# Kernel tuning notes

Hardware: AMD Instinct MI355X
Metric: run time of the kernel (lower is better)

Reference implementation:

```python
import jax, jax.numpy as jnp
import numpy as np

HID = 256

def lstm_cell(x, h, c, Wih, Whh, bih, bhh):
    # PyTorch LSTM gate order: i, f, g, o
    g = x @ Wih.T + h @ Whh.T + bih + bhh
    i, f, gg, o = jnp.split(g, 4, axis=-1)
    c = jax.nn.sigmoid(f) * c + jax.nn.sigmoid(i) * jnp.tanh(gg)
    h = jax.nn.sigmoid(o) * jnp.tanh(c)
    return h, c

def lstm_seq(x, Wih, Whh, bih, bhh):
    # x: [B, T, D] -> outputs [B, T, H], final (h, c)
    B = x.shape[0]
    h0 = jnp.zeros((B, HID), x.dtype)
    def step(carry, xt):
        h, c = lstm_cell(xt, carry[0], carry[1], Wih, Whh, bih, bhh)
        return (h, c), h
    (h, c), ys = jax.lax.scan(step, (h0, h0), jnp.swapaxes(x, 0, 1))
    return jnp.swapaxes(ys, 0, 1), h, c

def setup_inputs():
    key = jax.random.key(0)
    B, M, H_WIN, NTH, NTW = 512, 16, 25, 64, 64
    SAL = NTH * NTW
    ks = iter(jax.random.split(key, 40))
    def U(shape):
        return jax.random.uniform(next(ks), shape, jnp.float32, -0.0625, 0.0625)
    def lstm_p(pfx, din):
        return {pfx + '_Wih': U((4 * HID, din)), pfx + '_Whh': U((4 * HID, HID)),
                pfx + '_bih': U((4 * HID,)), pfx + '_bhh': U((4 * HID,))}
    inp = {
        'encoder_position_inputs': jax.random.normal(next(ks), (B, M, 3), jnp.float32) * 0.1,
        'encoder_saliency_inputs': jax.random.uniform(next(ks), (B, M, NTH, NTW), jnp.float32),
        'decoder_position_inputs': jax.random.normal(next(ks), (B, 1, 3), jnp.float32) * 0.1,
        'decoder_saliency_inputs': jax.random.uniform(next(ks), (B, H_WIN, NTH, NTW), jnp.float32),
    }
    for pfx, din in [('pe', 3), ('se', SAL), ('fe', 2 * HID), ('pd', 3), ('sd', SAL), ('fd', 2 * HID)]:
        inp.update(lstm_p(pfx, din))
    inp['f2_W'] = U((HID, HID)); inp['f2_b'] = U((HID,))
    inp['out_W'] = U((3, HID)); inp['out_b'] = U((3,))
    return inp

def reference(encoder_position_inputs, encoder_saliency_inputs, decoder_position_inputs, decoder_saliency_inputs,
              pe_Wih, pe_Whh, pe_bih, pe_bhh, se_Wih, se_Whh, se_bih, se_bhh,
              fe_Wih, fe_Whh, fe_bih, fe_bhh, pd_Wih, pd_Whh, pd_bih, pd_bhh,
              sd_Wih, sd_Whh, sd_bih, sd_bhh, fd_Wih, fd_Whh, fd_bih, fd_bhh,
              f2_W, f2_b, out_W, out_b):
    B, M = encoder_position_inputs.shape[:2]
    SAL = encoder_saliency_inputs.shape[2] * encoder_saliency_inputs.shape[3]
    # encoder
    out_pos, h1, c1 = lstm_seq(encoder_position_inputs, pe_Wih, pe_Whh, pe_bih, pe_bhh)
    out_sal, h2, c2 = lstm_seq(encoder_saliency_inputs.reshape(B, M, SAL), se_Wih, se_Whh, se_bih, se_bhh)
    conc_enc = jnp.concatenate([out_sal, out_pos], axis=-1)
    _, hf, cf = lstm_seq(conc_enc, fe_Wih, fe_Whh, fe_bih, fe_bhh)
    # decoder: H_WINDOW single-step recurrence; fuse LSTM restarts from (hf, cf) every step
    dec_sal = decoder_saliency_inputs.reshape(B, -1, SAL)
    def step(carry, sal_t):
        inp, h1, c1, h2, c2 = carry
        h1, c1 = lstm_cell(inp, h1, c1, pd_Wih, pd_Whh, pd_bih, pd_bhh)
        h2, c2 = lstm_cell(sal_t, h2, c2, sd_Wih, sd_Whh, sd_bih, sd_bhh)
        conc = jnp.concatenate([h2, h1], axis=-1)
        hfd, _ = lstm_cell(conc, hf, cf, fd_Wih, fd_Whh, fd_bih, fd_bhh)
        fuse2 = hfd @ f2_W.T + f2_b
        delta = fuse2 @ out_W.T + out_b
        pred = inp + delta  # toPosition: orientation + motion
        return (pred, h1, c1, h2, c2), pred
    init = (decoder_position_inputs[:, 0], h1, c1, h2, c2)
    _, preds = jax.lax.scan(step, init, jnp.swapaxes(dec_sal, 0, 1))
    return jnp.swapaxes(preds, 0, 1)  # [B, H_WINDOW, 3]
```

## Files before the change

### kernel.cpp

```cpp
#include <hip/hip_runtime.h>

#define HID 256
#define BATCH 512
#define MENC 16
#define HWIN 25
#define SALSZ 4096
#define BH (BATCH * HID)

typedef __attribute__((ext_vector_type(8))) short bf16x8;
typedef __attribute__((ext_vector_type(4))) float f32x4;

__device__ __forceinline__ float sigmf(float x) { return 1.0f / (1.0f + __expf(-x)); }
__device__ __forceinline__ ushort f2bf(float f) {
    uint32_t u = __float_as_uint(f);
    return (ushort)((u + 0x7fffu + ((u >> 16) & 1u)) >> 16);
}

#define GLOAD_LDS(gp, lp) \
    __builtin_amdgcn_global_load_lds((const __attribute__((address_space(1))) void*)(gp), \
                                     (__attribute__((address_space(3))) void*)(lp), 16, 0, 0)

__device__ __forceinline__ void st_u64(void* p, unsigned long long v) {
    __hip_atomic_store((unsigned long long*)p, v, __ATOMIC_RELAXED, __HIP_MEMORY_SCOPE_AGENT);
}

__device__ __forceinline__ void gbar_arrive(unsigned int* slot)
{
    __syncthreads();
    if (threadIdx.x == 0) atomicAdd(slot, 1u);
}
__device__ __forceinline__ void gbar_wait(unsigned int* slot, unsigned int nblk)
{
    if (threadIdx.x == 0) {
        while (__hip_atomic_load(slot, __ATOMIC_RELAXED, __HIP_MEMORY_SCOPE_AGENT) < nblk)
            __builtin_amdgcn_s_sleep(1);
    }
    __syncthreads();
}

__device__ __forceinline__ void stage_wtile(const ushort* Wsrc, int ldw, int u0,
                                            ushort* lds, int lane, int wq)
{
    const int sub = lane >> 5, uu = lane & 31;
#pragma unroll
    for (int i = 0; i < 8; ++i) {
        const int row = i * 8 + wq * 2 + sub;
        const int su  = uu ^ (row & 7);
        const int gr  = (row >> 4) * HID + u0 + (row & 15);
        GLOAD_LDS(Wsrc + (size_t)gr * ldw + su * 8, lds + i * 2048 + wq * 512);
    }
}

__device__ __forceinline__ void cell_g(const ushort* hrow0, int ldh,
                                       const ushort* WsL, f32x4 acc[4], int lane)
{
    const int fr = lane & 15, fq = lane >> 4;
    const ushort* hrow = hrow0 + (size_t)fr * ldh;
#pragma unroll
    for (int ks = 0; ks < 8; ++ks) {
        const bf16x8 af = *(const bf16x8*)(hrow + ks * 32 + fq * 8);
#pragma unroll
        for (int g = 0; g < 4; ++g) {
            const int vr = g * 16 + fr;
            const bf16x8 bf = *(const bf16x8*)(WsL + vr * 256 + (((ks * 4 + fq)) ^ (vr & 7)) * 8);
            acc[g] = __builtin_amdgcn_mfma_f32_16x16x32_bf16(af, bf, acc[g], 0, 0, 0);
        }
    }
}

struct Cvt9 {
    const float* s[9];
    ushort*      d[9];
    int          end[9];
};
__global__ __launch_bounds__(256)
void cvt_multi(Cvt9 A)
{
    int i = blockIdx.x * 256 + threadIdx.x;
    if (i >= A.end[8]) return;
    int seg = 0, beg = 0;
#pragma unroll
    for (int k = 0; k < 8; ++k)
        if (i >= A.end[k]) { seg = k + 1; beg = A.end[k]; }
    const int j = i - beg;
    const float4 v = *(const float4*)(A.s[seg] + (size_t)j * 4);
    *(ushort4*)(A.d[seg] + (size_t)j * 4) = make_ushort4(f2bf(v.x), f2bf(v.y), f2bf(v.z), f2bf(v.w));
}

__device__ __forceinline__ void loadA_f32(const float* Ag, int lda, int tid, float4 a[8])
{
    const int row_in = tid >> 3, ulin = tid & 7;
#pragma unroll
    for (int i = 0; i < 4; ++i) {
        const int row = i * 64 + row_in;
        const int su = (ulin ^ (row & 7)) * 8;
        a[2 * i + 0] = *(const float4*)(Ag + (size_t)row * lda + su);
        a[2 * i + 1] = *(const float4*)(Ag + (size_t)row * lda + su + 4);
    }
}
__device__ __forceinline__ void writeA_bf16(const float4 a[8], ushort* Al, int tid)
{
    const int row_in = tid >> 3, ulin = tid & 7;
#pragma unroll
    for (int i = 0; i < 4; ++i) {
        const int row = i * 64 + row_in;
        uint4 v;
        v.x = (uint)f2bf(a[2 * i].x) | ((uint)f2bf(a[2 * i].y) << 16);
        v.y = (uint)f2bf(a[2 * i].z) | ((uint)f2bf(a[2 * i].w) << 16);
        v.z = (uint)f2bf(a[2 * i + 1].x) | ((uint)f2bf(a[2 * i + 1].y) << 16);
        v.w = (uint)f2bf(a[2 * i + 1].z) | ((uint)f2bf(a[2 * i + 1].w) << 16);
        *(uint4*)(Al + row * 64 + ulin * 8) = v;
    }
}
__device__ __forceinline__ void stageB(const ushort* Bg, int ldw, ushort* Bl, int tid)
{
    const int row_in = tid >> 3, ulin = tid & 7;
#pragma unroll
    for (int i = 0; i < 4; ++i) {
        const int row = i * 64 + row_in;
        const int su = (ulin ^ (row & 7)) * 8;
        GLOAD_LDS(Bg + (size_t)row * ldw + su, Bl + row * 64 + ulin * 8);
    }
}

struct GemmJob { const float* A; const ushort* W; float* C; int nwg; };

__global__ __launch_bounds__(512, 2)
void gemm256f2(GemmJob j0, GemmJob j1)
{
    __shared__ ushort As[2][256 * 64];
    __shared__ ushort Bs[2][256 * 64];
    const int tid = threadIdx.x, lane = tid & 63, wid = tid >> 6;

    const GemmJob J = (blockIdx.x < (unsigned)j0.nwg) ? j0 : j1;
    int bid = (blockIdx.x < (unsigned)j0.nwg) ? blockIdx.x : blockIdx.x - j0.nwg;
    {
        const int nwg = J.nwg, q = nwg >> 3, r = nwg & 7;
        const int xcd = bid & 7, o = bid >> 3;
        bid = (xcd < r) ? xcd * (q + 1) + o : r * (q + 1) + (xcd - r) * q + o;
    }
    const int gx = 4;
    const int m0 = (bid / gx) * 256, n0 = (bid % gx) * 256;
    const int lda = SALSZ, ldw = SALSZ, ldc = 1024, K = SALSZ;

    const int wr = wid >> 2, wc = wid & 3;
    const int fr = lane & 15, fq = lane >> 4;

    f32x4 acc[8][4] = {};
    const int nt = K / 64;
    const float*  Ab0 = J.A + (size_t)m0 * lda;
    const ushort* Bb0 = J.W + (size_t)n0 * ldw;

    float4 ra[8];
    loadA_f32(Ab0, lda, tid, ra);
    stageB(Bb0, ldw, Bs[0], tid);
    writeA_bf16(ra, As[0], tid);
    loadA_f32(Ab0 + 64, lda, tid, ra);
    asm volatile("s_waitcnt vmcnt(8) lgkmcnt(0)" ::: "memory");
    __builtin_amdgcn_sched_barrier(0);
    __builtin_amdgcn_s_barrier();
    __builtin_amdgcn_sched_barrier(0);

    for (int t = 0; t < nt; ++t) {
        const int p = t & 1;
        const int t1 = (t + 1 < nt) ? t + 1 : nt - 1;
        const int t2 = (t + 2 < nt) ? t + 2 : nt - 1;
        stageB(Bb0 + t1 * 64, ldw, Bs[p ^ 1], tid);
        writeA_bf16(ra, As[p ^ 1], tid);
        loadA_f32(Ab0 + t2 * 64, lda, tid, ra);

        const ushort* Ab = As[p];
        const ushort* Bb = Bs[p];
#pragma unroll
        for (int ks = 0; ks < 2; ++ks) {
            bf16x8 bfr[4];
#pragma unroll
            for (int nf = 0; nf < 4; ++nf) {
                const int row = wc * 64 + nf * 16 + fr;
                bfr[nf] = *(const bf16x8*)(Bb + row * 64 + ((ks * 4 + fq) ^ (row & 7)) * 8);
            }
#pragma unroll
            for (int mh = 0; mh < 2; ++mh) {
                bf16x8 af[4];
#pragma unroll
                for (int i = 0; i < 4; ++i) {
                    const int row = wr * 128 + (mh * 4 + i) * 16 + fr;
                    af[i] = *(const bf16x8*)(Ab + row * 64 + ((ks * 4 + fq) ^ (row & 7)) * 8);
                }
                __builtin_amdgcn_s_setprio(1);
#pragma unroll
                for (int i = 0; i < 4; ++i)
#pragma unroll
                    for (int nf = 0; nf < 4; ++nf)
                        acc[mh * 4 + i][nf] = __builtin_amdgcn_mfma_f32_16x16x32_bf16(
                            af[i], bfr[nf], acc[mh * 4 + i][nf], 0, 0, 0);
                __builtin_amdgcn_s_setprio(0);
            }
        }
        if (t == nt - 1) break;
        asm volatile("s_waitcnt vmcnt(8) lgkmcnt(0)" ::: "memory");
        __builtin_amdgcn_sched_barrier(0);
        __builtin_amdgcn_s_barrier();
        __builtin_amdgcn_sched_barrier(0);
    }

    const int cl = lane & 15, ch = lane >> 4;
#pragma unroll
    for (int mf = 0; mf < 8; ++mf)
#pragma unroll
        for (int nf = 0; nf < 4; ++nf)
#pragma unroll
            for (int r = 0; r < 4; ++r)
                J.C[(size_t)(m0 + wr * 128 + mf * 16 + ch * 4 + r) * ldc
                    + n0 + wc * 64 + nf * 16 + cl] = acc[mf][nf][r];
}

__global__ __launch_bounds__(256)
void gemm_mfma_bt(const ushort* __restrict__ A, const ushort* __restrict__ W,
                  float* __restrict__ C, int M, int N, int K,
                  int lda, int ldw, int ldc, const float* __restrict__ rbias)
{
    __shared__ ushort As[128 * 32];
    __shared__ ushort Bs[128 * 32];
    const int t    = threadIdx.x;
    const int lane = t & 63, wid = t >> 6;
    const int m0 = blockIdx.y * 128, n0 = blockIdx.x * 128;
    const int wr = wid >> 1, wc = wid & 1;

    f32x4 acc[4][4] = {};

    const int sr = wid * 16 + (lane >> 2);
    const int su = ((lane & 3) ^ ((lane >> 3) & 3)) * 8;
    const ushort* Ag = A + (size_t)(m0 + sr) * lda + su;
    const ushort* Wg = W + (size_t)(n0 + sr) * ldw + su;
    ushort* Al = As + wid * 512;
    ushort* Bl = Bs + wid * 512;

    const int fr = lane & 15;
    const int fq = lane >> 4;
    const int sw = (fr >> 1) & 3;

    for (int k0 = 0; k0 < K; k0 += 32) {
        GLOAD_LDS(Ag,                    Al);
        GLOAD_LDS(Ag + (size_t)64 * lda, Al + 2048);
        GLOAD_LDS(Wg,                    Bl);
        GLOAD_LDS(Wg + (size_t)64 * ldw, Bl + 2048);
        Ag += 32; Wg += 32;
        __syncthreads();

        bf16x8 af[4], bfr[4];
#pragma unroll
        for (int m = 0; m < 4; ++m)
            af[m] = *(const bf16x8*)(As + (wr * 64 + m * 16 + fr) * 32 + (fq ^ sw) * 8);
#pragma unroll
        for (int n = 0; n < 4; ++n)
            bfr[n] = *(const bf16x8*)(Bs + (wc * 64 + n * 16 + fr) * 32 + (fq ^ sw) * 8);
#pragma unroll
        for (int m = 0; m < 4; ++m)
#pragma unroll
            for (int n = 0; n < 4; ++n)
                acc[m][n] = __builtin_amdgcn_mfma_f32_16x16x32_bf16(af[m], bfr[n], acc[m][n], 0, 0, 0);
        __syncthreads();
    }

    const int cl = lane & 15, ch = lane >> 4;
#pragma unroll
    for (int m = 0; m < 4; ++m)
#pragma unroll
        for (int n = 0; n < 4; ++n)
#pragma unroll
            for (int r = 0; r < 4; ++r) {
                const int mm = m0 + wr * 64 + m * 16 + ch * 4 + r;
                const int nn = n0 + wc * 64 + n * 16 + cl;
                float v = acc[m][n][r];
                if (rbias) v += rbias[(size_t)(mm & 511) * ldc + nn];
                C[(size_t)mm * ldc + nn] = v;
            }
}

__global__ __launch_bounds__(256)
void gemm_tn(const float* __restrict__ A, const float* __restrict__ W,
             const float* __restrict__ b1, const float* __restrict__ b2,
             float* __restrict__ C,
             int M, int N, int K, int lda, int ldw, int ldc)
{
    __shared__ float AsT[16][68];
    __shared__ float WsT[16][68];
    const int t  = threadIdx.x;
    const int tx = t & 15, ty = t >> 4;
    const int m0 = blockIdx.y * 64, n0 = blockIdx.x * 64;
    const int lr = t >> 2;
    const int c4 = t & 3;

    float acc[4][4];
#pragma unroll
    for (int i = 0; i < 4; ++i)
#pragma unroll
        for (int j = 0; j < 4; ++j) acc[i][j] = 0.0f;

    for (int k0 = 0; k0 < K; k0 += 16) {
        float a[4], w[4];
        const int kb = k0 + c4 * 4;
#pragma unroll
        for (int k = 0; k < 4; ++k) {
            a[k] = (kb + k < K) ? A[(size_t)(m0 + lr) * lda + kb + k] : 0.0f;
            w[k] = (kb + k < K) ? W[(size_t)(n0 + lr) * ldw + kb + k] : 0.0f;
        }
        __syncthreads();
#pragma unroll
        for (int k = 0; k < 4; ++k) {
            AsT[c4 * 4 + k][lr] = a[k];
            WsT[c4 * 4 + k][lr] = w[k];
        }
        __syncthreads();
#pragma unroll
        for (int kk = 0; kk < 16; ++kk) {
            const float4 av = *(const float4*)&AsT[kk][ty * 4];
            const float4 wv = *(const float4*)&WsT[kk][tx * 4];
            acc[0][0] += av.x * wv.x; acc[0][1] += av.x * wv.y; acc[0][2] += av.x * wv.z; acc[0][3] += av.x * wv.w;
            acc[1][0] += av.y * wv.x; acc[1][1] += av.y * wv.y; acc[1][2] += av.y * wv.z; acc[1][3] += av.y * wv.w;
            acc[2][0] += av.z * wv.x; acc[2][1] += av.z * wv.y; acc[2][2] += av.z * wv.z; acc[2][3] += av.z * wv.w;
            acc[3][0] += av.w * wv.x; acc[3][1] += av.w * wv.y; acc[3][2] += av.w * wv.z; acc[3][3] += av.w * wv.w;
        }
    }

#pragma unroll
    for (int i = 0; i < 4; ++i) {
        const int m = m0 + ty * 4 + i;
#pragma unroll
        for (int j = 0; j < 4; ++j) {
            const int n = n0 + tx * 4 + j;
            float v = acc[i][j];
            if (b1) v += b1[n];
            if (b2) v += b2[n];
            C[(size_t)m * ldc + n] = v;
        }
    }
}

struct EncArgs {
    const ushort *WHse, *WHpe;
    const float  *xg_se;
    const float  *enc_pos;
    const float  *se_b1, *se_b2, *pe_b1, *pe_b2;
    const float  *pe_Wih;
    ushort       *conc;
    float        *SE_C, *PE_C;
    unsigned int *bar;
};

__global__ __launch_bounds__(1024)
void enc_chain(EncArgs A)
{
    __shared__ ushort Ws[4][64 * 256];
    __shared__ ushort hloc[64][64];
    const int tid = threadIdx.x, lane = tid & 63, w = tid >> 6;
    const int role  = blockIdx.x >> 5;
    const int rem   = blockIdx.x & 31;
    const int btile = rem & 7, usup = rem >> 3;
    const int b0 = btile * 64, ub = usup * 64;
    const int usub = w & 3, bsub = w >> 2;
    const int u0t = ub + usub * 16;
    const int grp = role * 8 + btile;
    const int fr = lane & 15, fq = lane >> 4;
    const int u = u0t + fr;
    const int ul = usub * 16 + fr;
    const int coff = role ? 256 : 0;

    stage_wtile(role ? A.WHpe : A.WHse, HID, u0t, Ws[usub], lane, bsub);

    const float* b1 = role ? A.pe_b1 : A.se_b1;
    const float* b2 = role ? A.pe_b2 : A.se_b2;
    float bias[4], wxs[4][3];
#pragma unroll
    for (int g = 0; g < 4; ++g) {
        bias[g] = b1[g * HID + u] + b2[g * HID + u];
        wxs[g][0] = wxs[g][1] = wxs[g][2] = 0.0f;
        if (role) {
            wxs[g][0] = A.pe_Wih[(g * HID + u) * 3 + 0];
            wxs[g][1] = A.pe_Wih[(g * HID + u) * 3 + 1];
            wxs[g][2] = A.pe_Wih[(g * HID + u) * 3 + 2];
        }
    }
    float c[4] = {0.f, 0.f, 0.f, 0.f};
    __syncthreads();

    for (int t = 0; t < MENC; ++t) {
        float xg[4][4];
#pragma unroll
        for (int r = 0; r < 4; ++r) {
            const int b = b0 + bsub * 16 + fq * 4 + r;
            if (role) {
                const float* xp = A.enc_pos + ((size_t)b * MENC + t) * 3;
                xg[r][0] = xp[0]; xg[r][1] = xp[1]; xg[r][2] = xp[2]; xg[r][3] = 0.f;
            } else {
#pragma unroll
                for (int g = 0; g < 4; ++g)
                    xg[r][g] = A.xg_se[((size_t)b * MENC + t) * 1024 + g * HID + u];
            }
        }
        if (t > 0) gbar_wait(A.bar + grp * MENC + (t - 1), 4);
        f32x4 acc[4] = {};
        if (t > 0)
            cell_g(A.conc + ((size_t)(t - 1) * 512 + b0 + bsub * 16) * 512 + coff, 512,
                   Ws[usub], acc, lane);
#pragma unroll
        for (int r = 0; r < 4; ++r) {
            const int bl = bsub * 16 + fq * 4 + r;
            const int b = b0 + bl;
            float gv[4];
#pragma unroll
            for (int g = 0; g < 4; ++g) {
                float v = acc[g][r] + bias[g];
                if (role) v += xg[r][0] * wxs[g][0] + xg[r][1] * wxs[g][1] + xg[r][2] * wxs[g][2];
                else      v += xg[r][g];
                gv[g] = v;
            }
            const float cn = sigmf(gv[1]) * c[r] + sigmf(gv[0]) * tanhf(gv[2]);
            const float hn = sigmf(gv[3]) * tanhf(cn);
            c[r] = cn;
            hloc[bl][ul] = f2bf(hn);
            if (t == MENC - 1) (role ? A.PE_C : A.SE_C)[(size_t)b * HID + u] = cn;
        }
        __syncthreads();
        {
            const int row = tid >> 4, c8 = tid & 15;
            const unsigned long long v = *(const unsigned long long*)&hloc[row][c8 * 4];
            st_u64(A.conc + ((size_t)t * 512 + b0 + row) * 512 + coff + ub + c8 * 4, v);
        }
        if (t != MENC - 1) gbar_arrive(A.bar + grp * MENC + t);
    }
}

struct MidArgs {
    const ushort *WHsd, *WHfe;
    const float  *xg_sd;
    const float  *xg_fe;
    const float  *sd_b1, *sd_b2, *fe_b1, *fe_b2;
    const ushort *conc;
    const float  *SE_C;
    ushort       *SDB;
    ushort       *FEB;
    float        *FEH, *FE_C;
    unsigned int *bar;
};

__global__ __launch_bounds__(1024)
void mid_chain(MidArgs A)
{
    __shared__ ushort Ws[4][64 * 256];
    __shared__ ushort hloc[64][64];
    const int tid = threadIdx.x, lane = tid & 63, w = tid >> 6;
    const int role  = blockIdx.x >> 5;
    const int rem   = blockIdx.x & 31;
    const int btile = rem & 7, usup = rem >> 3;
    const int b0 = btile * 64, ub = usup * 64;
    const int usub = w & 3, bsub = w >> 2;
    const int u0t = ub + usub * 16;
    const int grp = role * 8 + btile;
    const int fr = lane & 15, fq = lane >> 4;
    const int u = u0t + fr;
    const int ul = usub * 16 + fr;
    const int NT = role ? MENC : HWIN;

    stage_wtile(role ? A.WHfe : A.WHsd, HID, u0t, Ws[usub], lane, bsub);

    const float* b1 = role ? A.fe_b1 : A.sd_b1;
    const float* b2 = role ? A.fe_b2 : A.sd_b2;
    float bias[4];
#pragma unroll
    for (int g = 0; g < 4; ++g) bias[g] = b1[g * HID + u] + b2[g * HID + u];

    float c[4];
#pragma unroll
    for (int r = 0; r < 4; ++r) {
        const int b = b0 + bsub * 16 + fq * 4 + r;
        c[r] = role ? 0.0f : A.SE_C[(size_t)b * HID + u];
    }
    __syncthreads();

    for (int t = 0; t < NT; ++t) {
        float xg[4][4];
#pragma unroll
        for (int r = 0; r < 4; ++r) {
            const int b = b0 + bsub * 16 + fq * 4 + r;
#pragma unroll
            for (int g = 0; g < 4; ++g)
                xg[r][g] = role ? A.xg_fe[((size_t)t * 512 + b) * 1024 + g * HID + u]
                                : A.xg_sd[((size_t)b * HWIN + t) * 1024 + g * HID + u];
        }
        if (t > 0) gbar_wait(A.bar + grp * HWIN + (t - 1), 4);
        f32x4 acc[4] = {};
        if (role == 0) {
            if (t == 0) cell_g(A.conc + ((size_t)15 * 512 + b0 + bsub * 16) * 512, 512,
                               Ws[usub], acc, lane);
            else        cell_g(A.SDB + ((size_t)(t - 1) * 512 + b0 + bsub * 16) * HID, HID,
                               Ws[usub], acc, lane);
        } else if (t > 0) {
            cell_g(A.FEB + ((size_t)(t - 1) * BATCH + b0 + bsub * 16) * HID, HID,
                   Ws[usub], acc, lane);
        }
#pragma unroll
        for (int r = 0; r < 4; ++r) {
            const int bl = bsub * 16 + fq * 4 + r;
            const int b = b0 + bl;
            float gv[4];
#pragma unroll
            for (int g = 0; g < 4; ++g)
                gv[g] = acc[g][r] + bias[g] + xg[r][g];
            const float cn = sigmf(gv[1]) * c[r] + sigmf(gv[0]) * tanhf(gv[2]);
            const float hn = sigmf(gv[3]) * tanhf(cn);
            c[r] = cn;
            hloc[bl][ul] = f2bf(hn);
            if (role == 1 && t == MENC - 1) {
                A.FEH[(size_t)b * HID + u] = hn;
                A.FE_C[(size_t)b * HID + u] = cn;
            }
        }
        __syncthreads();
        {
            const int row = tid >> 4, c8 = tid & 15;
            const unsigned long long v = *(const unsigned long long*)&hloc[row][c8 * 4];
            ushort* dst = role ? (A.FEB + ((size_t)t * BATCH + b0 + row) * 256 + ub + c8 * 4)
                               : (A.SDB + ((size_t)t * 512 + b0 + row) * 256 + ub + c8 * 4);
            st_u64(dst, v);
        }
        if (t != NT - 1) gbar_arrive(A.bar + grp * HWIN + t);
    }
}

struct DecArgs {
    const ushort *WHpd;
    const ushort *WFDh;
    const ushort *peF;
    const float  *PE_C, *FE_C;
    const float  *xh2;
    const float  *pd_b1, *pd_b2, *pd_Wih;
    const float  *G, *c3, *dec_pos;
    ushort       *H1;
    float        *DELTA;
    float        *out;
    unsigned int *bar;
};

__global__ __launch_bounds__(512)
void dec_chain(DecArgs A)
{
    __shared__ ushort Wpd[2][64 * 256], Wfd[2][64 * 256];
    __shared__ ushort hloc[64][32];
    __shared__ float pred_lds[192];
    const int tid = threadIdx.x, lane = tid & 63, w = tid >> 6;
    const int btile = blockIdx.x & 7, usup = blockIdx.x >> 3;
    const int b0 = btile * 64, ub = usup * 32;
    const int usub = w & 1, bsub = w >> 1;
    const int u0t = ub + usub * 16;
    const int fr = lane & 15, fq = lane >> 4;
    const int u = u0t + fr;
    const int ul = usub * 16 + fr;
    unsigned int* bars = A.bar + btile * 2 * HWIN;

    stage_wtile(A.WHpd, HID, u0t, Wpd[usub], lane, bsub);
    stage_wtile(A.WFDh, 512, u0t, Wfd[usub], lane, bsub);

    float pdb[4], wxs[4][3], cf[4], c1[4], Gu[3];
#pragma unroll
    for (int g = 0; g < 4; ++g) {
        pdb[g] = A.pd_b1[g * HID + u] + A.pd_b2[g * HID + u];
        wxs[g][0] = A.pd_Wih[(g * HID + u) * 3 + 0];
        wxs[g][1] = A.pd_Wih[(g * HID + u) * 3 + 1];
        wxs[g][2] = A.pd_Wih[(g * HID + u) * 3 + 2];
    }
#pragma unroll
    for (int r = 0; r < 4; ++r) {
        const int b = b0 + bsub * 16 + fq * 4 + r;
        c1[r] = A.PE_C[(size_t)b * HID + u];
        cf[r] = A.FE_C[(size_t)b * HID + u];
    }
    Gu[0] = A.G[0 * HID + u]; Gu[1] = A.G[1 * HID + u]; Gu[2] = A.G[2 * HID + u];
    const float c3r = (tid < 192) ? A.c3[tid % 3] : 0.0f;
    if (tid < 192) pred_lds[tid] = A.dec_pos[(size_t)(b0 + tid / 3) * 3 + tid % 3];
    __syncthreads();

    for (int t = 0; t < HWIN; ++t) {
        f32x4 acc[4] = {};
        if (t == 0) cell_g(A.peF + (size_t)(b0 + bsub * 16) * 512, 512, Wpd[usub], acc, lane);
        else        cell_g(A.H1 + ((size_t)(t - 1) * BATCH + b0 + bsub * 16) * HID, HID,
                           Wpd[usub], acc, lane);
        if (t > 0) {
            gbar_wait(bars + 2 * (t - 1) + 1, 8);
            if (tid < 192) {
                pred_lds[tid] += A.DELTA[((size_t)(t - 1) * 512 + b0 + tid / 3) * 3 + tid % 3] + c3r;
                if (usup == 0)
                    A.out[((size_t)(b0 + tid / 3) * HWIN + (t - 1)) * 3 + tid % 3] = pred_lds[tid];
            }
            __syncthreads();
        }
#pragma unroll
        for (int r = 0; r < 4; ++r) {
            const int bl = bsub * 16 + fq * 4 + r;
            const float x0 = pred_lds[bl * 3 + 0];
            const float x1 = pred_lds[bl * 3 + 1];
            const float x2 = pred_lds[bl * 3 + 2];
            float gv[4];
#pragma unroll
            for (int g = 0; g < 4; ++g)
                gv[g] = acc[g][r] + pdb[g] + x0 * wxs[g][0] + x1 * wxs[g][1] + x2 * wxs[g][2];
            const float cn = sigmf(gv[1]) * c1[r] + sigmf(gv[0]) * tanhf(gv[2]);
            const float hn = sigmf(gv[3]) * tanhf(cn);
            c1[r] = cn;
            hloc[bl][ul] = f2bf(hn);
        }
        __syncthreads();
        {
            const int row = tid >> 3, c8 = tid & 7;
            const unsigned long long v = *(const unsigned long long*)&hloc[row][c8 * 4];
            st_u64(A.H1 + ((size_t)t * BATCH + b0 + row) * 256 + ub + c8 * 4, v);
        }
        gbar_arrive(bars + 2 * t);
        float xh[4][4];
#pragma unroll
        for (int r = 0; r < 4; ++r) {
            const int b = b0 + bsub * 16 + fq * 4 + r;
#pragma unroll
            for (int g = 0; g < 4; ++g)
                xh[r][g] = A.xh2[((size_t)t * 512 + b) * 1024 + g * HID + u];
        }
        gbar_wait(bars + 2 * t, 8);
        {
            f32x4 accB[4] = {};
            cell_g(A.H1 + ((size_t)t * BATCH + b0 + bsub * 16) * HID, HID,
                   Wfd[usub], accB, lane);
#pragma unroll
            for (int r = 0; r < 4; ++r) {
                const int b = b0 + bsub * 16 + fq * 4 + r;
                float gv[4];
#pragma unroll
                for (int g = 0; g < 4; ++g)
                    gv[g] = accB[g][r] + xh[r][g];
                const float cn = sigmf(gv[1]) * cf[r] + sigmf(gv[0]) * tanhf(gv[2]);
                const float hn = sigmf(gv[3]) * tanhf(cn);
                float p0 = hn * Gu[0], p1 = hn * Gu[1], p2 = hn * Gu[2];
#pragma unroll
                for (int s = 1; s < 16; s <<= 1) {
                    p0 += __shfl_xor(p0, s);
                    p1 += __shfl_xor(p1, s);
                    p2 += __shfl_xor(p2, s);
                }
                if (fr == 0) {
                    float* d = A.DELTA + ((size_t)t * 512 + b) * 3;
                    atomicAdd(d + 0, p0); atomicAdd(d + 1, p1); atomicAdd(d + 2, p2);
                }
            }
        }
        gbar_arrive(bars + 2 * t + 1);
    }
    gbar_wait(bars + 2 * (HWIN - 1) + 1, 8);
    if (tid < 192) {
        pred_lds[tid] += A.DELTA[((size_t)(HWIN - 1) * 512 + b0 + tid / 3) * 3 + tid % 3] + c3r;
        if (usup == 0)
            A.out[((size_t)(b0 + tid / 3) * HWIN + (HWIN - 1)) * 3 + tid % 3] = pred_lds[tid];
    }
}

__global__ __launch_bounds__(256)
void precompute_G(const float* __restrict__ f2W, const float* __restrict__ f2b,
                  const float* __restrict__ outW, const float* __restrict__ outb,
                  float* __restrict__ G, float* __restrict__ c3)
{
    const int k = threadIdx.x;
    float g0 = 0.f, g1 = 0.f, g2 = 0.f;
    for (int n = 0; n < HID; ++n) {
        const float w = f2W[n * HID + k];
        g0 += outW[n] * w;
        g1 += outW[HID + n] * w;
        g2 += outW[2 * HID + n] * w;
    }
    G[k] = g0; G[HID + k] = g1; G[2 * HID + k] = g2;
    if (k < 3) {
        float s = outb[k];
        for (int n = 0; n < HID; ++n) s += outW[k * HID + n] * f2b[n];
        c3[k] = s;
    }
}

extern "C" void kernel_launch(void* const* d_in, const int* in_sizes, int n_in,
                              void* d_out, int out_size, void* d_ws, size_t ws_size,
                              hipStream_t stream)
{
    (void)in_sizes; (void)n_in; (void)out_size; (void)ws_size;
    const float* enc_pos = (const float*)d_in[0];
    const float* enc_sal = (const float*)d_in[1];
    const float* dec_pos = (const float*)d_in[2];
    const float* dec_sal = (const float*)d_in[3];
    const float *pe_Wih = (const float*)d_in[4],  *pe_Whh = (const float*)d_in[5],
                *pe_bih = (const float*)d_in[6],  *pe_bhh = (const float*)d_in[7];
    const float *se_Wih = (const float*)d_in[8],  *se_Whh = (const float*)d_in[9],
                *se_bih = (const float*)d_in[10], *se_bhh = (const float*)d_in[11];
    const float *fe_Wih = (const float*)d_in[12], *fe_Whh = (const float*)d_in[13],
                *fe_bih = (const float*)d_in[14], *fe_bhh = (const float*)d_in[15];
    const float *pd_Wih = (const float*)d_in[16], *pd_Whh = (const float*)d_in[17],
                *pd_bih = (const float*)d_in[18], *pd_bhh = (const float*)d_in[19];
    const float *sd_Wih = (const float*)d_in[20], *sd_Whh = (const float*)d_in[21],
                *sd_bih = (const float*)d_in[22], *sd_bhh = (const float*)d_in[23];
    const float *fd_Wih = (const float*)d_in[24], *fd_Whh = (const float*)d_in[25],
                *fd_bih = (const float*)d_in[26], *fd_bhh = (const float*)d_in[27];
    const float *f2_W = (const float*)d_in[28], *f2_b = (const float*)d_in[29];
    const float *out_W = (const float*)d_in[30], *out_b = (const float*)d_in[31];
    float* out = (float*)d_out;
    float* ws  = (float*)d_ws;

    size_t off = 0;
    float* XG_SE = ws + off; off += (size_t)8192 * 1024;
    float* XG_FE = ws + off; off += (size_t)8192 * 1024;
    float* BIG   = ws + off; off += (size_t)12800 * 1024;
    float* BIG2  = ws + off; off += (size_t)12800 * 1024;
    float* GBIAS = ws + off; off += (size_t)BATCH * 1024;
    float* PE_C  = ws + off; off += BH;
    float* SE_C  = ws + off; off += BH;
    float* FE_C  = ws + off; off += BH;
    float* FEH   = ws + off; off += BH;
    float* Gm    = ws + off; off += 1024;
    float* C3    = ws + off; off += 8;
    float* DELTA = ws + off; off += (size_t)HWIN * BATCH * 3 + 64;
    unsigned int* BAR = (unsigned int*)(ws + off); off += 1280;
    ushort* WSE  = (ushort*)(ws + off); off += ((size_t)1024 * 4096) / 2;
    ushort* WSD  = (ushort*)(ws + off); off += ((size_t)1024 * 4096) / 2;
    ushort* WFE  = (ushort*)(ws + off); off += ((size_t)1024 * 512) / 2;
    ushort* WFD  = (ushort*)(ws + off); off += ((size_t)1024 * 512) / 2;
    ushort* WHpe = (ushort*)(ws + off); off += ((size_t)1024 * 256) / 2;
    ushort* WHse = (ushort*)(ws + off); off += ((size_t)1024 * 256) / 2;
    ushort* WHfe = (ushort*)(ws + off); off += ((size_t)1024 * 256) / 2;
    ushort* WHsd = (ushort*)(ws + off); off += ((size_t)1024 * 256) / 2;
    ushort* WHpd = (ushort*)(ws + off); off += ((size_t)1024 * 256) / 2;
    ushort* CONC = (ushort*)(ws + off); off += ((size_t)MENC * 512 * 512) / 2;
    ushort* SDB  = (ushort*)(ws + off); off += ((size_t)HWIN * BH) / 2;
    ushort* FEB  = (ushort*)(ws + off); off += ((size_t)MENC * BH) / 2;
    ushort* H1   = (ushort*)(ws + off); off += ((size_t)HWIN * BH) / 2;

    hipMemsetAsync(DELTA, 0, ((size_t)HWIN * BATCH * 3 + 64 + 1280) * 4, stream);

    auto mgemm = [&](const ushort* A, const ushort* W, float* C,
                     int M, int N, int K, int lda, int ldw, int ldc, const float* rb) {
        gemm_mfma_bt<<<dim3(N / 128, M / 128), 256, 0, stream>>>(A, W, C, M, N, K, lda, ldw, ldc, rb);
    };

    {
        Cvt9 a;
        const float* srcs[9] = { se_Wih, sd_Wih, fe_Wih, fd_Wih, pe_Whh, se_Whh, fe_Whh, sd_Whh, pd_Whh };
        ushort*      dsts[9] = { WSE,    WSD,    WFE,    WFD,    WHpe,   WHse,   WHfe,   WHsd,   WHpd };
        const int    n4s[9]  = { 1024*4096/4, 1024*4096/4, 1024*512/4, 1024*512/4,
                                 1024*256/4, 1024*256/4, 1024*256/4, 1024*256/4, 1024*256/4 };
        int acc9 = 0;
        for (int i = 0; i < 9; ++i) { a.s[i] = srcs[i]; a.d[i] = dsts[i]; acc9 += n4s[i]; a.end[i] = acc9; }
        cvt_multi<<<(acc9 + 255) / 256, 256, 0, stream>>>(a);
    }
    precompute_G<<<1, 256, 0, stream>>>(f2_W, f2_b, out_W, out_b, Gm, C3);

    {
        GemmJob j0, j1;
        j0.A = enc_sal; j0.W = WSE; j0.C = XG_SE; j0.nwg = (8192 / 256) * 4;
        j1.A = dec_sal; j1.W = WSD; j1.C = BIG;   j1.nwg = (12800 / 256) * 4;
        gemm256f2<<<j0.nwg + j1.nwg, 512, 0, stream>>>(j0, j1);
    }

    {
        EncArgs a;
        a.WHse = WHse; a.WHpe = WHpe; a.xg_se = XG_SE; a.enc_pos = enc_pos;
        a.se_b1 = se_bih; a.se_b2 = se_bhh; a.pe_b1 = pe_bih; a.pe_b2 = pe_bhh;
        a.pe_Wih = pe_Wih; a.conc = CONC; a.SE_C = SE_C; a.PE_C = PE_C;
        a.bar = BAR;
        enc_chain<<<64, 1024, 0, stream>>>(a);
    }

    mgemm(CONC, WFE, XG_FE, 8192, 1024, 512, 512, 512, 1024, nullptr);

    {
        MidArgs a;
        a.WHsd = WHsd; a.WHfe = WHfe; a.xg_sd = BIG; a.xg_fe = XG_FE;
        a.sd_b1 = sd_bih; a.sd_b2 = sd_bhh; a.fe_b1 = fe_bih; a.fe_b2 = fe_bhh;
        a.conc = CONC; a.SE_C = SE_C; a.SDB = SDB; a.FEB = FEB;
        a.FEH = FEH; a.FE_C = FE_C; a.bar = BAR + 256;
        mid_chain<<<64, 1024, 0, stream>>>(a);
    }

    gemm_tn<<<dim3(16, 8), 256, 0, stream>>>(FEH, fd_Whh, fd_bih, fd_bhh, GBIAS,
                                             BATCH, 1024, HID, HID, HID, 1024);
    mgemm(SDB, WFD, BIG2, 12800, 1024, HID, HID, 512, 1024, GBIAS);

    {
        DecArgs a;
        a.WHpd = WHpd; a.WFDh = WFD + 256;
        a.peF = CONC + ((size_t)15 * 512) * 512 + 256;
        a.PE_C = PE_C; a.FE_C = FE_C; a.xh2 = BIG2;
        a.pd_b1 = pd_bih; a.pd_b2 = pd_bhh; a.pd_Wih = pd_Wih;
        a.G = Gm; a.c3 = C3; a.dec_pos = dec_pos;
        a.H1 = H1; a.DELTA = DELTA; a.out = out; a.bar = BAR + 656;
        dec_chain<<<64, 512, 0, stream>>>(a);
    }
}
```

Measured before the change: 1.176 ms.

## Shrink big saliency GEMM tile to 256x128 with K-step 32 for higher occupancy

Reworks the fused fp32-A/bf16-W saliency input-projection GEMM to use 256x128 output tiles and a K-step of 32 instead of 256x256 and 64. LDS use per block drops, launch bounds allow 4 blocks per CU instead of 2, and the grid doubles to spread work across more CUs. The swizzle pattern and warp layout are adapted to the narrower LDS rows. In exchange there is less data reuse per tile, more A re-reads from global memory (A is loaded once per N tile), and twice as many barriers per unit of K.

```diff
diff --git a/kernel.cpp b/kernel.cpp
--- a/kernel.cpp
+++ b/kernel.cpp
@@ -87,49 +87,45 @@
     *(ushort4*)(A.d[seg] + (size_t)j * 4) = make_ushort4(f2bf(v.x), f2bf(v.y), f2bf(v.z), f2bf(v.w));
 }
 
-__device__ __forceinline__ void loadA_f32(const float* Ag, int lda, int tid, float4 a[8])
-{
-    const int row_in = tid >> 3, ulin = tid & 7;
-#pragma unroll
-    for (int i = 0; i < 4; ++i) {
-        const int row = i * 64 + row_in;
-        const int su = (ulin ^ (row & 7)) * 8;
-        a[2 * i + 0] = *(const float4*)(Ag + (size_t)row * lda + su);
-        a[2 * i + 1] = *(const float4*)(Ag + (size_t)row * lda + su + 4);
-    }
-}
-__device__ __forceinline__ void writeA_bf16(const float4 a[8], ushort* Al, int tid)
-{
-    const int row_in = tid >> 3, ulin = tid & 7;
-#pragma unroll
-    for (int i = 0; i < 4; ++i) {
-        const int row = i * 64 + row_in;
+__device__ __forceinline__ void loadA32(const float* Ag, int lda, int tid, float4 ra[4])
+{
+    const int row = tid >> 1, ub = tid & 1;
+#pragma unroll
+    for (int i = 0; i < 2; ++i) {
+        const int u = ub + i * 2;
+        const int su = u ^ ((row >> 1) & 3);
+        ra[2 * i + 0] = *(const float4*)(Ag + (size_t)row * lda + su * 8);
+        ra[2 * i + 1] = *(const float4*)(Ag + (size_t)row * lda + su * 8 + 4);
+    }
+}
+__device__ __forceinline__ void writeA32(const float4 ra[4], ushort* Al, int tid)
+{
+    const int row = tid >> 1, ub = tid & 1;
+#pragma unroll
+    for (int i = 0; i < 2; ++i) {
+        const int u = ub + i * 2;
         uint4 v;
-        v.x = (uint)f2bf(a[2 * i].x) | ((uint)f2bf(a[2 * i].y) << 16);
-        v.y = (uint)f2bf(a[2 * i].z) | ((uint)f2bf(a[2 * i].w) << 16);
-        v.z = (uint)f2bf(a[2 * i + 1].x) | ((uint)f2bf(a[2 * i + 1].y) << 16);
-        v.w = (uint)f2bf(a[2 * i + 1].z) | ((uint)f2bf(a[2 * i + 1].w) << 16);
-        *(uint4*)(Al + row * 64 + ulin * 8) = v;
-    }
-}
-__device__ __forceinline__ void stageB(const ushort* Bg, int ldw, ushort* Bl, int tid)
-{
-    const int row_in = tid >> 3, ulin = tid & 7;
-#pragma unroll
-    for (int i = 0; i < 4; ++i) {
-        const int row = i * 64 + row_in;
-        const int su = (ulin ^ (row & 7)) * 8;
-        GLOAD_LDS(Bg + (size_t)row * ldw + su, Bl + row * 64 + ulin * 8);
-    }
+        v.x = (uint)f2bf(ra[2 * i].x) | ((uint)f2bf(ra[2 * i].y) << 16);
+        v.y = (uint)f2bf(ra[2 * i].z) | ((uint)f2bf(ra[2 * i].w) << 16);
+        v.z = (uint)f2bf(ra[2 * i + 1].x) | ((uint)f2bf(ra[2 * i + 1].y) << 16);
+        v.w = (uint)f2bf(ra[2 * i + 1].z) | ((uint)f2bf(ra[2 * i + 1].w) << 16);
+        *(uint4*)(Al + row * 32 + u * 8) = v;
+    }
+}
+__device__ __forceinline__ void stageB32(const ushort* Bg, int ldw, ushort* Bl, int tid)
+{
+    const int row = tid >> 2, u = tid & 3;
+    const int su = u ^ ((row >> 1) & 3);
+    GLOAD_LDS(Bg + (size_t)row * ldw + su * 8, Bl + row * 32 + u * 8);
 }
 
 struct GemmJob { const float* A; const ushort* W; float* C; int nwg; };
 
-__global__ __launch_bounds__(512, 2)
+__global__ __launch_bounds__(512, 4)
 void gemm256f2(GemmJob j0, GemmJob j1)
 {
-    __shared__ ushort As[2][256 * 64];
-    __shared__ ushort Bs[2][256 * 64];
+    __shared__ ushort As[2][256 * 32];
+    __shared__ ushort Bs[2][128 * 32];
     const int tid = threadIdx.x, lane = tid & 63, wid = tid >> 6;
 
     const GemmJob J = (blockIdx.x < (unsigned)j0.nwg) ? j0 : j1;
@@ -139,24 +135,24 @@
         const int xcd = bid & 7, o = bid >> 3;
         bid = (xcd < r) ? xcd * (q + 1) + o : r * (q + 1) + (xcd - r) * q + o;
     }
-    const int gx = 4;
-    const int m0 = (bid / gx) * 256, n0 = (bid % gx) * 256;
+    const int gx = 8;
+    const int m0 = (bid / gx) * 256, n0 = (bid % gx) * 128;
     const int lda = SALSZ, ldw = SALSZ, ldc = 1024, K = SALSZ;
 
-    const int wr = wid >> 2, wc = wid & 3;
+    const int wr = wid >> 1, wc = wid & 1;
     const int fr = lane & 15, fq = lane >> 4;
 
-    f32x4 acc[8][4] = {};
-    const int nt = K / 64;
+    f32x4 acc[4][4] = {};
+    const int nt = K / 32;
     const float*  Ab0 = J.A + (size_t)m0 * lda;
     const ushort* Bb0 = J.W + (size_t)n0 * ldw;
 
-    float4 ra[8];
-    loadA_f32(Ab0, lda, tid, ra);
-    stageB(Bb0, ldw, Bs[0], tid);
-    writeA_bf16(ra, As[0], tid);
-    loadA_f32(Ab0 + 64, lda, tid, ra);
-    asm volatile("s_waitcnt vmcnt(8) lgkmcnt(0)" ::: "memory");
+    float4 ra[4];
+    loadA32(Ab0, lda, tid, ra);
+    stageB32(Bb0, ldw, Bs[0], tid);
+    writeA32(ra, As[0], tid);
+    loadA32(Ab0 + 32, lda, tid, ra);
+    asm volatile("s_waitcnt vmcnt(4) lgkmcnt(0)" ::: "memory");
     __builtin_amdgcn_sched_barrier(0);
     __builtin_amdgcn_s_barrier();
     __builtin_amdgcn_sched_barrier(0);
@@ -165,40 +161,35 @@
         const int p = t & 1;
         const int t1 = (t + 1 < nt) ? t + 1 : nt - 1;
         const int t2 = (t + 2 < nt) ? t + 2 : nt - 1;
-        stageB(Bb0 + t1 * 64, ldw, Bs[p ^ 1], tid);
-        writeA_bf16(ra, As[p ^ 1], tid);
-        loadA_f32(Ab0 + t2 * 64, lda, tid, ra);
+        stageB32(Bb0 + t1 * 32, ldw, Bs[p ^ 1], tid);
+        writeA32(ra, As[p ^ 1], tid);
+        loadA32(Ab0 + t2 * 32, lda, tid, ra);
 
         const ushort* Ab = As[p];
         const ushort* Bb = Bs[p];
-#pragma unroll
-        for (int ks = 0; ks < 2; ++ks) {
-            bf16x8 bfr[4];
-#pragma unroll
-            for (int nf = 0; nf < 4; ++nf) {
-                const int row = wc * 64 + nf * 16 + fr;
-                bfr[nf] = *(const bf16x8*)(Bb + row * 64 + ((ks * 4 + fq) ^ (row & 7)) * 8);
-            }
-#pragma unroll
-            for (int mh = 0; mh < 2; ++mh) {
-                bf16x8 af[4];
-#pragma unroll
-                for (int i = 0; i < 4; ++i) {
-                    const int row = wr * 128 + (mh * 4 + i) * 16 + fr;
-                    af[i] = *(const bf16x8*)(Ab + row * 64 + ((ks * 4 + fq) ^ (row & 7)) * 8);
-                }
-                __builtin_amdgcn_s_setprio(1);
-#pragma unroll
-                for (int i = 0; i < 4; ++i)
-#pragma unroll
-                    for (int nf = 0; nf < 4; ++nf)
-                        acc[mh * 4 + i][nf] = __builtin_amdgcn_mfma_f32_16x16x32_bf16(
-                            af[i], bfr[nf], acc[mh * 4 + i][nf], 0, 0, 0);
-                __builtin_amdgcn_s_setprio(0);
-            }
-        }
+        bf16x8 bfr[4];
+#pragma unroll
+        for (int nf = 0; nf < 4; ++nf) {
+            const int row = wc * 64 + nf * 16 + fr;
+            bfr[nf] = *(const bf16x8*)(Bb + row * 32 + (fq ^ ((row >> 1) & 3)) * 8);
+        }
+        bf16x8 af[4];
+#pragma unroll
+        for (int mf = 0; mf < 4; ++mf) {
+            const int row = wr * 64 + mf * 16 + fr;
+            af[mf] = *(const bf16x8*)(Ab + row * 32 + (fq ^ ((row >> 1) & 3)) * 8);
+        }
+        __builtin_amdgcn_s_setprio(1);
+#pragma unroll
+        for (int mf = 0; mf < 4; ++mf)
+#pragma unroll
+            for (int nf = 0; nf < 4; ++nf)
+                acc[mf][nf] = __builtin_amdgcn_mfma_f32_16x16x32_bf16(
+                    af[mf], bfr[nf], acc[mf][nf], 0, 0, 0);
+        __builtin_amdgcn_s_setprio(0);
+
         if (t == nt - 1) break;
-        asm volatile("s_waitcnt vmcnt(8) lgkmcnt(0)" ::: "memory");
+        asm volatile("s_waitcnt vmcnt(4) lgkmcnt(0)" ::: "memory");
         __builtin_amdgcn_sched_barrier(0);
         __builtin_amdgcn_s_barrier();
         __builtin_amdgcn_sched_barrier(0);
@@ -206,12 +197,12 @@
 
     const int cl = lane & 15, ch = lane >> 4;
 #pragma unroll
-    for (int mf = 0; mf < 8; ++mf)
+    for (int mf = 0; mf < 4; ++mf)
 #pragma unroll
         for (int nf = 0; nf < 4; ++nf)
 #pragma unroll
             for (int r = 0; r < 4; ++r)
-                J.C[(size_t)(m0 + wr * 128 + mf * 16 + ch * 4 + r) * ldc
+                J.C[(size_t)(m0 + wr * 64 + mf * 16 + ch * 4 + r) * ldc
                     + n0 + wc * 64 + nf * 16 + cl] = acc[mf][nf][r];
 }
 
@@ -758,8 +749,8 @@
 
     {
         GemmJob j0, j1;
-        j0.A = enc_sal; j0.W = WSE; j0.C = XG_SE; j0.nwg = (8192 / 256) * 4;
-        j1.A = dec_sal; j1.W = WSD; j1.C = BIG;   j1.nwg = (12800 / 256) * 4;
+        j0.A = enc_sal; j0.W = WSE; j0.C = XG_SE; j0.nwg = (8192 / 256) * 8;
+        j1.A = dec_sal; j1.W = WSD; j1.C = BIG;   j1.nwg = (12800 / 256) * 8;
         gemm256f2<<<j0.nwg + j1.nwg, 512, 0, stream>>>(j0, j1);
     }
 
```

After: 1.212 ms. 3.1% more time.
